# Optimization experiments

Hardware: AMD Instinct MI355X
Metric: run time of the kernel (lower is better)

The kernel has to match this reference:

```python
import jax, jax.numpy as jnp
from jax import lax
import numpy as np

B, C, L = 8, 64, 32768
K = 4
DEPTH = 8


def _causal_depthwise_conv(x, weight, dilation):
    # x: [B, C, L], weight: [C, 1, K] depthwise (groups=C). stride=1 so the
    # torch pad formula reduces to left-pad dilation*(K-1), output length L.
    pad = dilation * (K - 1)
    return lax.conv_general_dilated(
        x, weight,
        window_strides=(1,),
        padding=[(pad, 0)],
        rhs_dilation=(dilation,),
        dimension_numbers=("NCH", "OIH", "NCH"),
        feature_group_count=C,
    )


def setup_inputs() -> dict:
    key = jax.random.key(0)
    k1, k2, k3, k4 = jax.random.split(key, 4)
    scalar = np.sqrt(2.0 / (K * 2)).astype(np.float32)
    w_scale = np.sqrt(2.0 / (2 * DEPTH + 4)).astype(np.float32)
    return {
        "x": jax.random.normal(k1, (B, C, L), dtype=jnp.float32),
        "h0": jax.random.uniform(k2, (C, 1, K), minval=-1.0, maxval=1.0, dtype=jnp.float32) * scalar,
        "h1": jax.random.uniform(k3, (C, 1, K), minval=-1.0, maxval=1.0, dtype=jnp.float32) * scalar,
        "w": jax.random.uniform(k4, (C, DEPTH + 2), minval=-1.0, maxval=1.0, dtype=jnp.float32) * w_scale,
    }


def reference(x, h0, h1, w):
    residual_low = x
    y = jnp.zeros_like(x)
    dilation = 1
    for i in range(DEPTH, 0, -1):
        residual_high = _causal_depthwise_conv(residual_low, h1, dilation)
        residual_low = _causal_depthwise_conv(residual_low, h0, dilation)
        y = y + w[:, i][None, :, None] * residual_high
        dilation *= 2
    y = y + w[:, 0][None, :, None] * residual_low
    y = y + x * w[:, -1][None, :, None]
    # dropout p=0 is identity; torch GELU default is exact (erf)
    return jax.nn.gelu(y, approximate=False)
```

## Files before the change

### kernel.cpp

```cpp
#include <hip/hip_runtime.h>
#include <cmath>

namespace {

typedef _Float16 h8 __attribute__((ext_vector_type(8)));
typedef _Float16 h2 __attribute__((ext_vector_type(2)));
typedef __fp16   fp2 __attribute__((ext_vector_type(2)));

constexpr int C_     = 64;
constexpr int L_     = 32768;
constexpr int TILE   = 4096;
constexpr int HALO   = 776;
constexpr int NB     = TILE + HALO;
constexpr int NU     = NB / 8;
constexpr int HALO_U = HALO / 8;
constexpr int NT     = L_ / TILE;
constexpr int BLK    = 256;
constexpr int S2N    = NU - 2 * BLK;

__device__ __forceinline__ h8 ld8(const _Float16* p) { return *reinterpret_cast<const h8*>(p); }
__device__ __forceinline__ void st8(_Float16* p, h8 v) { *reinterpret_cast<h8*>(p) = v; }
__device__ __forceinline__ float4 ld4f(const float* p) { return *reinterpret_cast<const float4*>(p); }
__device__ __forceinline__ void st4f(float* p, float4 v) { *reinterpret_cast<float4*>(p) = v; }
__device__ __forceinline__ h8 sp8(_Float16 v) { return (h8){v,v,v,v,v,v,v,v}; }

__device__ __forceinline__ h8 fma8(h8 a, h8 b, h8 c) {
    return __builtin_elementwise_fma(a, b, c);
}

template<int K>
__device__ __forceinline__ h8 shconc(h8 A, h8 B) {
    return __builtin_shufflevector(A, B, K, K+1, K+2, K+3, K+4, K+5, K+6, K+7);
}

__device__ __forceinline__ h2 pkrtz(float lo, float hi) {
    const fp2 r = __builtin_amdgcn_cvt_pkrtz(lo, hi);
    return __builtin_bit_cast(h2, r);
}
__device__ __forceinline__ h8 pack8(float4 a, float4 b) {
    const h2 p0 = pkrtz(a.x, a.y);
    const h2 p1 = pkrtz(a.z, a.w);
    const h2 p2 = pkrtz(b.x, b.y);
    const h2 p3 = pkrtz(b.z, b.w);
    return (h8){p0[0], p0[1], p1[0], p1[1], p2[0], p2[1], p3[0], p3[1]};
}

__device__ __forceinline__ float gelu_f(float v) {
    const float z = v * (1.5957691216057308f + 0.0713548162726f * v * v);
    const float e = __expf(-z);
    return v * __builtin_amdgcn_rcpf(1.0f + e);
}

__device__ __forceinline__ h8 dot_nl(const h8 T0, const h8 T1, const h8 T2,
                                     const h8 T3, const _Float16* c) {
    h8 nl = sp8(c[0]) * T0;
    nl = fma8(sp8(c[1]), T1, nl);
    nl = fma8(sp8(c[2]), T2, nl);
    nl = fma8(sp8(c[3]), T3, nl);
    return nl;
}
__device__ __forceinline__ void dot_acc(const h8 T0, const h8 T1, const h8 T2,
                                        const h8 T3, const _Float16* c, h8& yv) {
    h8 yt = yv;
    yt = fma8(sp8(c[0]), T0, yt);
    yt = fma8(sp8(c[1]), T1, yt);
    yt = fma8(sp8(c[2]), T2, yt);
    yt = fma8(sp8(c[3]), T3, yt);
    yv = yt;
}

template<int D, bool LAST>
__device__ __forceinline__ void unit_step(const _Float16* __restrict__ src,
                                          _Float16* __restrict__ dst, int un,
                                          h8& lwv, h8& yv, bool doY,
                                          const _Float16* c1, const _Float16* c0)
{
    const int p = 8 * un;
    const h8 T3 = lwv;
    h8 T0, T1, T2;
    if constexpr (D == 2) {
        const h8 Lv = ld8(&src[p - 8]);
        T0 = shconc<2>(Lv, T3); T1 = shconc<4>(Lv, T3); T2 = shconc<6>(Lv, T3);
    } else if constexpr (D == 4) {
        const h8 Lv = ld8(&src[p - 8]);
        const h8 LL = ld8(&src[p - 16]);
        T0 = shconc<4>(LL, Lv); T1 = Lv; T2 = shconc<4>(Lv, T3);
    } else {
        T0 = ld8(&src[p - 3 * D]);
        T1 = ld8(&src[p - 2 * D]);
        T2 = ld8(&src[p - D]);
    }
    if (doY) dot_acc(T0, T1, T2, T3, c1, yv);
    const h8 nl = dot_nl(T0, T1, T2, T3, c0);
    if constexpr (LAST) {
        yv += nl;
    } else {
        lwv = nl;
        st8(&dst[p], nl);
    }
}

template<int D, int STARTU, bool LAST>
__device__ __forceinline__ void level_pass(const _Float16* __restrict__ src,
                                           _Float16* __restrict__ dst,
                                           const _Float16* h0h, const _Float16* h1h,
                                           _Float16 wih, _Float16 w0h,
                                           h8* lw, h8* yacc, int tid)
{
    _Float16 c1[4], c0[4];
#pragma unroll
    for (int t = 0; t < 4; ++t) {
        c1[t] = wih * h1h[t];
        c0[t] = LAST ? (_Float16)(w0h * h0h[t]) : h0h[t];
    }
    unit_step<D, LAST>(src, dst, tid + BLK, lw[1], yacc[1], true, c1, c0);
    if (tid < S2N)
        unit_step<D, LAST>(src, dst, tid + 2 * BLK, lw[2], yacc[2], true, c1, c0);
    if (tid >= STARTU)
        unit_step<D, LAST>(src, dst, tid, lw[0], yacc[0], tid >= HALO_U, c1, c0);
}

__global__ __launch_bounds__(BLK, 8)
void cmrc_kernel(const float* __restrict__ x,
                 const float* __restrict__ h0,
                 const float* __restrict__ h1,
                 const float* __restrict__ w,
                 float* __restrict__ out)
{
    __shared__ alignas(16) _Float16 buf[2][NB];

    const int tid  = threadIdx.x;
    const int blk  = blockIdx.x;
    const int tile = blk % NT;
    const int bc   = blk / NT;
    const int c    = bc % C_;
    const long row = (long)bc * L_;
    const int  t0  = tile * TILE - HALO;

    _Float16 h0h[4], h1h[4];
#pragma unroll
    for (int k = 0; k < 4; ++k) {
        h0h[k] = (_Float16)h0[c * 4 + k];
        h1h[k] = (_Float16)h1[c * 4 + k];
    }
    _Float16 wh[10];
#pragma unroll
    for (int i = 0; i < 10; ++i) wh[i] = (_Float16)w[c * 10 + i];

    _Float16 c18[4];
#pragma unroll
    for (int t = 0; t < 4; ++t) c18[t] = wh[8] * h1h[t];

    h8 lw[3];
    h8 yacc[3];

#pragma unroll
    for (int u = 0; u < 3; ++u) {
        yacc[u] = sp8((_Float16)0.f);
        const int un = tid + u * BLK;
        if (un < NU) {
            const int p = 8 * un;
            const int t = t0 + p;
            float4 xa = make_float4(0.f, 0.f, 0.f, 0.f), xb = xa;
            float4 xm1 = xa, xm2 = xa;
            if (t >= 0) { xa = ld4f(&x[row + t]);     xb = ld4f(&x[row + t + 4]); }
            if (t >= 8) { xm1 = ld4f(&x[row + t - 8]); xm2 = ld4f(&x[row + t - 4]); }
            const h8 X0 = pack8(xa, xb);
            const h8 Xm = pack8(xm1, xm2);
            const h8 A0 = shconc<5>(Xm, X0);
            const h8 A1 = shconc<6>(Xm, X0);
            const h8 A2 = shconc<7>(Xm, X0);
            const h8 l1 = dot_nl(A0, A1, A2, X0, h0h);
            st8(&buf[0][p], l1);
            lw[u] = l1;
            if (un >= HALO_U) {
                h8 yv = sp8(wh[9]) * X0;
                dot_acc(A0, A1, A2, X0, c18, yv);
                yacc[u] = yv;
            }
        }
    }
    __syncthreads();

    level_pass<2,   2,  false>(buf[0], buf[1], h0h, h1h, wh[7], (_Float16)0.f, lw, yacc, tid); __syncthreads();
    level_pass<4,   4,  false>(buf[1], buf[0], h0h, h1h, wh[6], (_Float16)0.f, lw, yacc, tid); __syncthreads();
    level_pass<8,   7,  false>(buf[0], buf[1], h0h, h1h, wh[5], (_Float16)0.f, lw, yacc, tid); __syncthreads();
    level_pass<16,  13, false>(buf[1], buf[0], h0h, h1h, wh[4], (_Float16)0.f, lw, yacc, tid); __syncthreads();
    level_pass<32,  25, false>(buf[0], buf[1], h0h, h1h, wh[3], (_Float16)0.f, lw, yacc, tid); __syncthreads();
    level_pass<64,  49, false>(buf[1], buf[0], h0h, h1h, wh[2], (_Float16)0.f, lw, yacc, tid); __syncthreads();
    level_pass<128, 97, true >(buf[0], buf[1], h0h, h1h, wh[1], wh[0],         lw, yacc, tid);

#pragma unroll
    for (int u = 0; u < 3; ++u) {
        const int un = tid + u * BLK;
        if (un >= HALO_U && un < NU) {
            const int p = 8 * un;
            const h8 v = yacc[u];
            float4 oa, ob;
            oa.x = gelu_f((float)v[0]); oa.y = gelu_f((float)v[1]);
            oa.z = gelu_f((float)v[2]); oa.w = gelu_f((float)v[3]);
            ob.x = gelu_f((float)v[4]); ob.y = gelu_f((float)v[5]);
            ob.z = gelu_f((float)v[6]); ob.w = gelu_f((float)v[7]);
            st4f(&out[row + t0 + p], oa);
            st4f(&out[row + t0 + p + 4], ob);
        }
    }
}

}

extern "C" void kernel_launch(void* const* d_in, const int* in_sizes, int n_in,
                              void* d_out, int out_size, void* d_ws, size_t ws_size,
                              hipStream_t stream)
{
    const float* x  = (const float*)d_in[0];
    const float* h0 = (const float*)d_in[1];
    const float* h1 = (const float*)d_in[2];
    const float* w  = (const float*)d_in[3];
    float* out = (float*)d_out;

    const int nblocks = (out_size / L_) * NT;
    cmrc_kernel<<<nblocks, BLK, 0, stream>>>(x, h0, h1, w, out);
}
```

Baseline: 40.99 us.

## Use single-wavefront blocks with smaller tiles and in-place LDS buffer

Shrinks each tile from 4096 to 2048 samples and each block from 256 to 64 threads, so one wavefront handles a whole tile with six units per lane. The ping-pong LDS buffers become a single in-place buffer. Lanes walk their units from high to low index, so writes land above positions still to be read. The intent is cheaper barriers within one wave, less LDS per block and more resident blocks. The cost is a larger share of redundant halo recomputation (776 halo samples against a smaller tile), and correctness now depends on the in-place read/write ordering within the wave.

```diff
diff --git a/kernel.cpp b/kernel.cpp
--- a/kernel.cpp
+++ b/kernel.cpp
@@ -9,14 +9,14 @@
 
 constexpr int C_     = 64;
 constexpr int L_     = 32768;
-constexpr int TILE   = 4096;
+constexpr int TILE   = 2048;
 constexpr int HALO   = 776;
 constexpr int NB     = TILE + HALO;
 constexpr int NU     = NB / 8;
 constexpr int HALO_U = HALO / 8;
 constexpr int NT     = L_ / TILE;
-constexpr int BLK    = 256;
-constexpr int S2N    = NU - 2 * BLK;
+constexpr int BLK    = 64;
+constexpr int UMAX   = 6;
 
 __device__ __forceinline__ h8 ld8(const _Float16* p) { return *reinterpret_cast<const h8*>(p); }
 __device__ __forceinline__ void st8(_Float16* p, h8 v) { *reinterpret_cast<h8*>(p) = v; }
@@ -69,40 +69,8 @@
     yv = yt;
 }
 
-template<int D, bool LAST>
-__device__ __forceinline__ void unit_step(const _Float16* __restrict__ src,
-                                          _Float16* __restrict__ dst, int un,
-                                          h8& lwv, h8& yv, bool doY,
-                                          const _Float16* c1, const _Float16* c0)
-{
-    const int p = 8 * un;
-    const h8 T3 = lwv;
-    h8 T0, T1, T2;
-    if constexpr (D == 2) {
-        const h8 Lv = ld8(&src[p - 8]);
-        T0 = shconc<2>(Lv, T3); T1 = shconc<4>(Lv, T3); T2 = shconc<6>(Lv, T3);
-    } else if constexpr (D == 4) {
-        const h8 Lv = ld8(&src[p - 8]);
-        const h8 LL = ld8(&src[p - 16]);
-        T0 = shconc<4>(LL, Lv); T1 = Lv; T2 = shconc<4>(Lv, T3);
-    } else {
-        T0 = ld8(&src[p - 3 * D]);
-        T1 = ld8(&src[p - 2 * D]);
-        T2 = ld8(&src[p - D]);
-    }
-    if (doY) dot_acc(T0, T1, T2, T3, c1, yv);
-    const h8 nl = dot_nl(T0, T1, T2, T3, c0);
-    if constexpr (LAST) {
-        yv += nl;
-    } else {
-        lwv = nl;
-        st8(&dst[p], nl);
-    }
-}
-
 template<int D, int STARTU, bool LAST>
-__device__ __forceinline__ void level_pass(const _Float16* __restrict__ src,
-                                           _Float16* __restrict__ dst,
+__device__ __forceinline__ void level_pass(_Float16* __restrict__ buf,
                                            const _Float16* h0h, const _Float16* h1h,
                                            _Float16 wih, _Float16 w0h,
                                            h8* lw, h8* yacc, int tid)
@@ -113,21 +81,45 @@
         c1[t] = wih * h1h[t];
         c0[t] = LAST ? (_Float16)(w0h * h0h[t]) : h0h[t];
     }
-    unit_step<D, LAST>(src, dst, tid + BLK, lw[1], yacc[1], true, c1, c0);
-    if (tid < S2N)
-        unit_step<D, LAST>(src, dst, tid + 2 * BLK, lw[2], yacc[2], true, c1, c0);
-    if (tid >= STARTU)
-        unit_step<D, LAST>(src, dst, tid, lw[0], yacc[0], tid >= HALO_U, c1, c0);
-}
-
-__global__ __launch_bounds__(BLK, 8)
+#pragma unroll
+    for (int uu = UMAX - 1; uu >= 0; --uu) {
+        const int un = tid + uu * BLK;
+        if (un >= STARTU && un < NU) {
+            const int p = 8 * un;
+            const h8 T3 = lw[uu];
+            h8 T0, T1, T2;
+            if constexpr (D == 2) {
+                const h8 Lv = ld8(&buf[p - 8]);
+                T0 = shconc<2>(Lv, T3); T1 = shconc<4>(Lv, T3); T2 = shconc<6>(Lv, T3);
+            } else if constexpr (D == 4) {
+                const h8 Lv = ld8(&buf[p - 8]);
+                const h8 LL = ld8(&buf[p - 16]);
+                T0 = shconc<4>(LL, Lv); T1 = Lv; T2 = shconc<4>(Lv, T3);
+            } else {
+                T0 = ld8(&buf[p - 3 * D]);
+                T1 = ld8(&buf[p - 2 * D]);
+                T2 = ld8(&buf[p - D]);
+            }
+            if (un >= HALO_U) dot_acc(T0, T1, T2, T3, c1, yacc[uu]);
+            const h8 nl = dot_nl(T0, T1, T2, T3, c0);
+            if constexpr (LAST) {
+                yacc[uu] += nl;
+            } else {
+                lw[uu] = nl;
+                st8(&buf[p], nl);
+            }
+        }
+    }
+}
+
+__global__ __launch_bounds__(BLK, 5)
 void cmrc_kernel(const float* __restrict__ x,
                  const float* __restrict__ h0,
                  const float* __restrict__ h1,
                  const float* __restrict__ w,
                  float* __restrict__ out)
 {
-    __shared__ alignas(16) _Float16 buf[2][NB];
+    __shared__ alignas(16) _Float16 buf[NB];
 
     const int tid  = threadIdx.x;
     const int blk  = blockIdx.x;
@@ -151,27 +143,27 @@
 #pragma unroll
     for (int t = 0; t < 4; ++t) c18[t] = wh[8] * h1h[t];
 
-    h8 lw[3];
-    h8 yacc[3];
-
-#pragma unroll
-    for (int u = 0; u < 3; ++u) {
+    h8 lw[UMAX];
+    h8 yacc[UMAX];
+
+#pragma unroll
+    for (int u = 0; u < UMAX; ++u) {
         yacc[u] = sp8((_Float16)0.f);
         const int un = tid + u * BLK;
         if (un < NU) {
             const int p = 8 * un;
             const int t = t0 + p;
-            float4 xa = make_float4(0.f, 0.f, 0.f, 0.f), xb = xa;
-            float4 xm1 = xa, xm2 = xa;
-            if (t >= 0) { xa = ld4f(&x[row + t]);     xb = ld4f(&x[row + t + 4]); }
-            if (t >= 8) { xm1 = ld4f(&x[row + t - 8]); xm2 = ld4f(&x[row + t - 4]); }
+            const float4 z4 = make_float4(0.f, 0.f, 0.f, 0.f);
+            float4 xa = z4, xb = z4, xm1 = z4, xm2 = z4;
+            if (t >= 0) { xa  = ld4f(&x[row + t]);      xb  = ld4f(&x[row + t + 4]); }
+            if (t >= 8) { xm1 = ld4f(&x[row + t - 8]);  xm2 = ld4f(&x[row + t - 4]); }
             const h8 X0 = pack8(xa, xb);
             const h8 Xm = pack8(xm1, xm2);
             const h8 A0 = shconc<5>(Xm, X0);
             const h8 A1 = shconc<6>(Xm, X0);
             const h8 A2 = shconc<7>(Xm, X0);
             const h8 l1 = dot_nl(A0, A1, A2, X0, h0h);
-            st8(&buf[0][p], l1);
+            st8(&buf[p], l1);
             lw[u] = l1;
             if (un >= HALO_U) {
                 h8 yv = sp8(wh[9]) * X0;
@@ -182,16 +174,16 @@
     }
     __syncthreads();
 
-    level_pass<2,   2,  false>(buf[0], buf[1], h0h, h1h, wh[7], (_Float16)0.f, lw, yacc, tid); __syncthreads();
-    level_pass<4,   4,  false>(buf[1], buf[0], h0h, h1h, wh[6], (_Float16)0.f, lw, yacc, tid); __syncthreads();
-    level_pass<8,   7,  false>(buf[0], buf[1], h0h, h1h, wh[5], (_Float16)0.f, lw, yacc, tid); __syncthreads();
-    level_pass<16,  13, false>(buf[1], buf[0], h0h, h1h, wh[4], (_Float16)0.f, lw, yacc, tid); __syncthreads();
-    level_pass<32,  25, false>(buf[0], buf[1], h0h, h1h, wh[3], (_Float16)0.f, lw, yacc, tid); __syncthreads();
-    level_pass<64,  49, false>(buf[1], buf[0], h0h, h1h, wh[2], (_Float16)0.f, lw, yacc, tid); __syncthreads();
-    level_pass<128, 97, true >(buf[0], buf[1], h0h, h1h, wh[1], wh[0],         lw, yacc, tid);
-
-#pragma unroll
-    for (int u = 0; u < 3; ++u) {
+    level_pass<2,   2,  false>(buf, h0h, h1h, wh[7], (_Float16)0.f, lw, yacc, tid); __syncthreads();
+    level_pass<4,   4,  false>(buf, h0h, h1h, wh[6], (_Float16)0.f, lw, yacc, tid); __syncthreads();
+    level_pass<8,   7,  false>(buf, h0h, h1h, wh[5], (_Float16)0.f, lw, yacc, tid); __syncthreads();
+    level_pass<16,  13, false>(buf, h0h, h1h, wh[4], (_Float16)0.f, lw, yacc, tid); __syncthreads();
+    level_pass<32,  25, false>(buf, h0h, h1h, wh[3], (_Float16)0.f, lw, yacc, tid); __syncthreads();
+    level_pass<64,  49, false>(buf, h0h, h1h, wh[2], (_Float16)0.f, lw, yacc, tid); __syncthreads();
+    level_pass<128, 97, true >(buf, h0h, h1h, wh[1], wh[0],         lw, yacc, tid);
+
+#pragma unroll
+    for (int u = 0; u < UMAX; ++u) {
         const int un = tid + u * BLK;
         if (un >= HALO_U && un < NU) {
             const int p = 8 * un;
```

Result: slower. 70.88 us (+72.9%).
